# Performance work log

Hardware: AMD Instinct MI355X
Metric: run time of the kernel (lower is better)

The kernel has to match this reference:

```python
import jax, jax.numpy as jnp
import numpy as np

OT_GAMMA = 1.0
OT_EPS = 1e-06
OT_ITER = 20
L2_EPS = 1e-12  # F.normalize default eps


def _forward(ft, fs):
    # X = cat(ft, fs): [2n, d]
    X = jnp.concatenate([ft, fs], axis=0)
    # cosine similarity (F.normalize p=2 along dim=1, then X Xn^T)
    Xn = X / jnp.maximum(jnp.linalg.norm(X, axis=1, keepdims=True), L2_EPS)
    C = Xn @ Xn.T  # [2n, 2n]
    n = C.shape[0] // 2
    M = C[:n, n:]  # teacher-student cross block [n, n]
    # zscore_normalize (torch.std is unbiased -> ddof=1)
    M = (M - M.mean()) / jnp.std(M, ddof=1)

    # sinkhorn(1 - M[None], gamma, eps, maxiters), logspace=False, r=c=None
    Mb = (1.0 - M)[None, :, :]  # [1, n, n]
    B, H, W = Mb.shape
    r = 1.0 / H
    c = 1.0 / W
    P0 = jnp.exp(-OT_GAMMA * (Mb - jnp.min(Mb, axis=2, keepdims=True)))

    def step(carry, _):
        P, done = carry
        alpha = P.sum(axis=2, keepdims=True)        # [B, H, 1]
        P1 = P / alpha * r                          # row-normalize
        beta = P1.sum(axis=1, keepdims=True)        # [B, 1, W]
        new_done = done | (jnp.max(jnp.abs(beta - c)) <= OT_EPS)
        # torch breaks AFTER row-normalization when converged
        P2 = jnp.where(new_done, P1, P1 / beta * c)
        P_next = jnp.where(done, P, P2)             # freeze once converged
        return (P_next, new_done), None

    (P, _), _ = jax.lax.scan(step, (P0, jnp.array(False)), None, length=OT_ITER)
    P = P[0]  # squeeze batch -> [n, n]

    # doubly_normalize
    P = P / P.sum(axis=1, keepdims=True)
    P = P / P.sum(axis=0, keepdims=True)

    # torch.norm(A, 2) with no dim flattens -> Frobenius norm
    I = jnp.eye(P.shape[1], dtype=P.dtype)
    loss_ot = jnp.linalg.norm(P - I)
    return loss_ot, P, M


def setup_inputs() -> dict:
    key = jax.random.key(0)
    k1, k2 = jax.random.split(key)
    ft = jax.random.normal(k1, (4096, 1024), dtype=jnp.float32)
    fs = jax.random.normal(k2, (4096, 1024), dtype=jnp.float32)
    return {"ft": ft, "fs": fs}


def reference(ft, fs):
    return _forward(ft, fs)
```

## Files before the change

### kernel.cpp

```cpp
#include <hip/hip_runtime.h>
#include <stdint.h>
#include <math.h>


#define NN 4096
#define DIM 1024
#define OT_ITERS 20
#define OT_EPS_F 1e-6f
#define RC (1.0f/4096.0f)
#define RPB 16
#define SBT 512

typedef __bf16 bf16_t;
typedef _Float16 half_t;
typedef __bf16 bf16x8 __attribute__((ext_vector_type(8)));
typedef _Float16 halfx8 __attribute__((ext_vector_type(8)));
typedef float floatx4 __attribute__((ext_vector_type(4)));

typedef __attribute__((address_space(1))) void gv_t;
typedef __attribute__((address_space(3))) void lv_t;

__device__ __forceinline__ void gld_lds16(const void* g, void* lds_uniform) {
  uint32_t loff = (uint32_t)(uintptr_t)lds_uniform;
  loff = (uint32_t)__builtin_amdgcn_readfirstlane((int)loff);
  __builtin_amdgcn_global_load_lds((gv_t*)(uintptr_t)g, (lv_t*)(uintptr_t)loff, 16, 0, 0);
}

__device__ __forceinline__ void gbar(uint32_t* bar, uint32_t g) {
  __syncthreads();
  if (threadIdx.x == 0) {
    uint32_t* cnt = bar + ((blockIdx.x >> 5) * 64);
    uint32_t* root = bar + 512;
    uint32_t* gen = bar + 576;
    if (__hip_atomic_fetch_add(cnt, 1u, __ATOMIC_RELEASE, __HIP_MEMORY_SCOPE_AGENT) == 31u) {
      __hip_atomic_store(cnt, 0u, __ATOMIC_RELAXED, __HIP_MEMORY_SCOPE_AGENT);
      if (__hip_atomic_fetch_add(root, 1u, __ATOMIC_ACQ_REL, __HIP_MEMORY_SCOPE_AGENT) == 7u) {
        __hip_atomic_store(root, 0u, __ATOMIC_RELAXED, __HIP_MEMORY_SCOPE_AGENT);
        __hip_atomic_store(gen, g, __ATOMIC_RELEASE, __HIP_MEMORY_SCOPE_AGENT);
      }
    }
    while (__hip_atomic_load(gen, __ATOMIC_RELAXED, __HIP_MEMORY_SCOPE_AGENT) < g)
      __builtin_amdgcn_s_sleep(1);
    __builtin_amdgcn_fence(__ATOMIC_ACQUIRE, "agent");
  }
  __syncthreads();
}

__global__ __launch_bounds__(256) void norm_rows2(const float* __restrict__ ft,
                                                  const float* __restrict__ fs,
                                                  bf16_t* __restrict__ A,
                                                  bf16_t* __restrict__ B,
                                                  uint32_t* __restrict__ bar) {
  int gb = blockIdx.x;
  const float* X = (gb < 1024) ? ft : fs;
  bf16_t* Y = (gb < 1024) ? A : B;
  int bb = gb & 1023;
  int tid = threadIdx.x;
  int wave = tid >> 6, lane = tid & 63;
  int row = bb * 4 + wave;
  const float* xr = X + (size_t)row * DIM;
  float xv[16];
  float ss = 0.f;
#pragma unroll
  for (int k = 0; k < 16; k++) { xv[k] = xr[lane + 64 * k]; ss += xv[k] * xv[k]; }
#pragma unroll
  for (int off = 1; off < 64; off <<= 1) ss += __shfl_xor(ss, off, 64);
  float inv = rsqrtf(ss);
  bf16_t* yr = Y + (size_t)row * DIM;
#pragma unroll
  for (int k = 0; k < 16; k++) yr[lane + 64 * k] = (bf16_t)(xv[k] * inv);
  if (gb == 0) {
    for (int i = tid; i < 640; i += 256) bar[i] = 0u;
  }
}

__global__ __launch_bounds__(256) void gemm_bt(const bf16_t* __restrict__ A,
                                               const bf16_t* __restrict__ B,
                                               float* __restrict__ C,
                                               float* __restrict__ sumArr,
                                               float* __restrict__ sqArr,
                                               float* __restrict__ rmPart) {
  __shared__ __align__(16) bf16_t As[2][128 * 32];
  __shared__ __align__(16) bf16_t Bs[2][128 * 32];
  __shared__ float sred[8];
  int tid = threadIdx.x;
  int wave = tid >> 6, lane = tid & 63;
  int quad = lane >> 4, l16 = lane & 15;
  int bm = blockIdx.y, bn = blockIdx.x;
  int waveM = wave >> 1, waveN = wave & 1;
  floatx4 acc[4][4] = {};

  auto stage = [&](int k0, int buf) {
#pragma unroll
    for (int t = 0; t < 2; t++) {
      int cbase = t * 256 + wave * 64;
      int c = cbase + lane;
      int row = c >> 2, kc = c & 3;
      gld_lds16(A + (size_t)(bm * 128 + row) * DIM + (k0 + kc * 8),
                (char*)&As[buf][0] + (size_t)cbase * 16);
      gld_lds16(B + (size_t)(bn * 128 + row) * DIM + (k0 + kc * 8),
                (char*)&Bs[buf][0] + (size_t)cbase * 16);
    }
  };

  stage(0, 0);
  asm volatile("s_waitcnt vmcnt(0)" ::: "memory");
  __builtin_amdgcn_s_barrier();
  int cur = 0;
  for (int k0 = 0; k0 < DIM; k0 += 32) {
    if (k0 + 32 < DIM) stage(k0 + 32, cur ^ 1);
    bf16x8 af[4], bfr[4];
#pragma unroll
    for (int mt = 0; mt < 4; mt++)
      af[mt] = *(const bf16x8*)(&As[cur][0] + (waveM * 64 + mt * 16 + l16) * 32 + quad * 8);
#pragma unroll
    for (int nt = 0; nt < 4; nt++)
      bfr[nt] = *(const bf16x8*)(&Bs[cur][0] + (waveN * 64 + nt * 16 + l16) * 32 + quad * 8);
#pragma unroll
    for (int mt = 0; mt < 4; mt++)
#pragma unroll
      for (int nt = 0; nt < 4; nt++)
        acc[mt][nt] = __builtin_amdgcn_mfma_f32_16x16x32_bf16(af[mt], bfr[nt], acc[mt][nt], 0, 0, 0);
    asm volatile("s_waitcnt vmcnt(0)" ::: "memory");
    __builtin_amdgcn_s_barrier();
    cur ^= 1;
  }

  float lsum = 0.f, lsq = 0.f;
#pragma unroll
  for (int mt = 0; mt < 4; mt++) {
#pragma unroll
    for (int r = 0; r < 4; r++) {
      int gi = bm * 128 + waveM * 64 + mt * 16 + quad * 4 + r;
      float rmax = -3.4e38f;
#pragma unroll
      for (int nt = 0; nt < 4; nt++) {
        float vv = acc[mt][nt][r];
        int gj = bn * 128 + waveN * 64 + nt * 16 + l16;
        C[(size_t)gi * NN + gj] = vv;
        lsum += vv;
        lsq += vv * vv;
        rmax = fmaxf(rmax, vv);
      }
#pragma unroll
      for (int off = 1; off < 16; off <<= 1) rmax = fmaxf(rmax, __shfl_xor(rmax, off, 64));
      if (l16 == 0) rmPart[(size_t)(bn * 2 + waveN) * NN + gi] = rmax;
    }
  }
#pragma unroll
  for (int off = 1; off < 64; off <<= 1) {
    lsum += __shfl_xor(lsum, off, 64);
    lsq += __shfl_xor(lsq, off, 64);
  }
  if (lane == 0) { sred[wave] = lsum; sred[4 + wave] = lsq; }
  __syncthreads();
  if (tid == 0) {
    int bid = bm * 32 + bn;
    sumArr[bid] = sred[0] + sred[1] + sred[2] + sred[3];
    sqArr[bid] = sred[4] + sred[5] + sred[6] + sred[7];
  }
}

__global__ __launch_bounds__(256) void row_stats(const float* __restrict__ sumArr,
                                                 const float* __restrict__ sqArr,
                                                 const float* __restrict__ rmPart,
                                                 float* __restrict__ rowmax,
                                                 float* __restrict__ scal) {
  int tid = threadIdx.x;
  int row = blockIdx.x * 256 + tid;
  float rm = -3.4e38f;
#pragma unroll 8
  for (int p = 0; p < 64; p++) rm = fmaxf(rm, rmPart[(size_t)p * NN + row]);
  rowmax[row] = rm;
  if (blockIdx.x == 0) {
    double ds = (double)sumArr[tid] + (double)sumArr[tid + 256] +
                (double)sumArr[tid + 512] + (double)sumArr[tid + 768];
    double dq = (double)sqArr[tid] + (double)sqArr[tid + 256] +
                (double)sqArr[tid + 512] + (double)sqArr[tid + 768];
#pragma unroll
    for (int off = 1; off < 64; off <<= 1) {
      ds += __shfl_xor(ds, off, 64);
      dq += __shfl_xor(dq, off, 64);
    }
    __shared__ double dr[8];
    int wave = tid >> 6, lane = tid & 63;
    if (lane == 0) { dr[wave] = ds; dr[4 + wave] = dq; }
    __syncthreads();
    if (tid == 0) {
      double sum = dr[0] + dr[1] + dr[2] + dr[3];
      double sumsq = dr[4] + dr[5] + dr[6] + dr[7];
      double Nd = (double)NN * (double)NN;
      double meand = sum / Nd;
      double var = (sumsq - sum * sum / Nd) / (Nd - 1.0);
      scal[2] = (float)meand;
      scal[3] = (float)(1.0 / sqrt(var));
    }
  }
}

__global__ __launch_bounds__(SBT, 2) void sinkhorn_full(
    float* __restrict__ Mraw,
    float* __restrict__ Mstd,
    const float* __restrict__ scal,
    const float* __restrict__ rowmax,
    float* __restrict__ u,
    float* __restrict__ t,
    float* __restrict__ s,
    float* __restrict__ lossArr,
    uint32_t* __restrict__ bar,
    float* __restrict__ out) {
  __shared__ float red[8 * RPB];
  __shared__ float u_lds[RPB];
  __shared__ float rowmax_l[RPB];
  __shared__ float mdred[8];

  const int b = blockIdx.x;
  const int tid = threadIdx.x;
  const int wave = tid >> 6, lane = tid & 63;
  const int g0 = b * RPB;
  const int c0 = tid * 8;
  const int r0 = tid * 8;
  uint32_t bg = 0;
  const float mean = scal[2], istd = scal[3];

  halfx8 kcol[16];
  {
    float rmx[8];
    *(float4*)&rmx[0] = *(const float4*)(rowmax + r0);
    *(float4*)&rmx[4] = *(const float4*)(rowmax + r0 + 4);
#pragma unroll
    for (int rl = 0; rl < 8; rl++) {
      const float* mr = Mraw + (size_t)(r0 + rl) * NN + g0;
      float v16[16];
      *(float4*)&v16[0] = *(const float4*)(mr);
      *(float4*)&v16[4] = *(const float4*)(mr + 4);
      *(float4*)&v16[8] = *(const float4*)(mr + 8);
      *(float4*)&v16[12] = *(const float4*)(mr + 12);
      float rm = rmx[rl];
      halfx8 lo, hi;
#pragma unroll
      for (int q = 0; q < 8; q++) {
        lo[q] = (half_t)__expf((v16[q] - rm) * istd);
        hi[q] = (half_t)__expf((v16[8 + q] - rm) * istd);
      }
      kcol[rl * 2] = lo;
      kcol[rl * 2 + 1] = hi;
    }
  }

  if (tid < RPB) rowmax_l[tid] = rowmax[g0 + tid];
  __syncthreads();
  halfx8 kreg[RPB];
#pragma unroll
  for (int i = 0; i < RPB; i++) {
    float rm = rowmax_l[i];
    const float* mr = Mraw + (size_t)(g0 + i) * NN + c0;
    float* mo = Mstd + (size_t)(g0 + i) * NN + c0;
    float4 a = *(const float4*)mr;
    float4 bb = *(const float4*)(mr + 4);
    float4 sa, sb;
    sa.x = (a.x - mean) * istd;  sa.y = (a.y - mean) * istd;
    sa.z = (a.z - mean) * istd;  sa.w = (a.w - mean) * istd;
    sb.x = (bb.x - mean) * istd; sb.y = (bb.y - mean) * istd;
    sb.z = (bb.z - mean) * istd; sb.w = (bb.w - mean) * istd;
    *(float4*)mo = sa;
    *(float4*)(mo + 4) = sb;
    halfx8 kp;
    kp[0] = (half_t)__expf((a.x - rm) * istd);
    kp[1] = (half_t)__expf((a.y - rm) * istd);
    kp[2] = (half_t)__expf((a.z - rm) * istd);
    kp[3] = (half_t)__expf((a.w - rm) * istd);
    kp[4] = (half_t)__expf((bb.x - rm) * istd);
    kp[5] = (half_t)__expf((bb.y - rm) * istd);
    kp[6] = (half_t)__expf((bb.z - rm) * istd);
    kp[7] = (half_t)__expf((bb.w - rm) * istd);
    kreg[i] = kp;
  }

  float vr[8];
#pragma unroll
  for (int q = 0; q < 8; q++) vr[q] = 1.0f;

  auto row_phase = [&](float scale, bool toLds) {
    float part[RPB];
#pragma unroll
    for (int i = 0; i < RPB; i++) {
      float p = 0.f;
#pragma unroll
      for (int q = 0; q < 8; q++) p += (float)kreg[i][q] * vr[q];
      part[i] = p;
    }
#pragma unroll
    for (int off = 1; off < 64; off <<= 1)
#pragma unroll
      for (int i = 0; i < RPB; i++) part[i] += __shfl_xor(part[i], off, 64);
    if (lane == 0) {
#pragma unroll
      for (int i = 0; i < RPB; i++) red[wave * RPB + i] = part[i];
    }
    __syncthreads();
    if (tid < RPB) {
      float dsum = 0.f;
#pragma unroll
      for (int w = 0; w < 8; w++) dsum += red[w * RPB + tid];
      float uv = scale / dsum;
      u[g0 + tid] = uv;
      if (toLds) u_lds[tid] = uv;
    }
  };

  auto col_phase = [&](float* dst) {
    float u8[8];
    *(float4*)&u8[0] = *(const float4*)(u + r0);
    *(float4*)&u8[4] = *(const float4*)(u + r0 + 4);
    float tp[RPB];
#pragma unroll
    for (int j = 0; j < RPB; j++) tp[j] = 0.f;
#pragma unroll
    for (int rl = 0; rl < 8; rl++) {
      float uv = u8[rl];
#pragma unroll
      for (int q = 0; q < 8; q++) {
        tp[q] += (float)kcol[rl * 2][q] * uv;
        tp[8 + q] += (float)kcol[rl * 2 + 1][q] * uv;
      }
    }
#pragma unroll
    for (int off = 1; off < 64; off <<= 1)
#pragma unroll
      for (int j = 0; j < RPB; j++) tp[j] += __shfl_xor(tp[j], off, 64);
    if (lane == 0) {
#pragma unroll
      for (int j = 0; j < RPB; j++) red[wave * RPB + j] = tp[j];
    }
    __syncthreads();
    if (tid < RPB) {
      float tv = 0.f;
#pragma unroll
      for (int w = 0; w < 8; w++) tv += red[w * RPB + tid];
      dst[g0 + tid] = tv;
    }
  };

  auto mdcheck = [&](float* t8) -> float {
    *(float4*)&t8[0] = *(const float4*)(t + c0);
    *(float4*)&t8[4] = *(const float4*)(t + c0 + 4);
    float dev = 0.f;
#pragma unroll
    for (int q = 0; q < 8; q++) dev = fmaxf(dev, fabsf(vr[q] * t8[q] - RC));
#pragma unroll
    for (int off = 1; off < 64; off <<= 1) dev = fmaxf(dev, __shfl_xor(dev, off, 64));
    if (lane == 0) mdred[wave] = dev;
    __syncthreads();
    float md = mdred[0];
#pragma unroll
    for (int w = 1; w < 8; w++) md = fmaxf(md, mdred[w]);
    __syncthreads();
    return md;
  };

  bool frozen = false;
  for (int it = 0; it < OT_ITERS; it++) {
    if (it > 0) {
      float t8[8];
      float md = mdcheck(t8);
      if (md <= OT_EPS_F) { frozen = true; break; }
#pragma unroll
      for (int q = 0; q < 8; q++) vr[q] = RC / t8[q];
    }
    row_phase(RC, false);
    gbar(bar, ++bg);
    col_phase(t);
    gbar(bar, ++bg);
  }
  if (!frozen) {
    float t8[8];
    float md = mdcheck(t8);
    if (md > OT_EPS_F) {
#pragma unroll
      for (int q = 0; q < 8; q++) vr[q] = RC / t8[q];
    }
  }

  row_phase(1.0f, true);
  gbar(bar, ++bg);
  col_phase(s);
  gbar(bar, ++bg);

  float s8[8];
  *(float4*)&s8[0] = *(const float4*)(s + c0);
  *(float4*)&s8[4] = *(const float4*)(s + c0 + 4);
  float isv[8];
#pragma unroll
  for (int q = 0; q < 8; q++) isv[q] = 1.0f / s8[q];
  float ls = 0.f;
#pragma unroll
  for (int i = 0; i < RPB; i++) {
    int gi = g0 + i;
    float wi = u_lds[i];
    float* prow = Mraw + (size_t)gi * NN + c0;
    float4 pa, pb;
    float pv[8];
#pragma unroll
    for (int q = 0; q < 8; q++) {
      float p = (float)kreg[i][q] * wi * isv[q];
      pv[q] = p;
      float d = p - ((gi == c0 + q) ? 1.0f : 0.0f);
      ls += d * d;
    }
    pa.x = pv[0]; pa.y = pv[1]; pa.z = pv[2]; pa.w = pv[3];
    pb.x = pv[4]; pb.y = pv[5]; pb.z = pv[6]; pb.w = pv[7];
    *(float4*)prow = pa;
    *(float4*)(prow + 4) = pb;
  }
#pragma unroll
  for (int off = 1; off < 64; off <<= 1) ls += __shfl_xor(ls, off, 64);
  if (lane == 0) red[wave] = ls;
  __syncthreads();
  if (tid == 0) {
    float tot = 0.f;
#pragma unroll
    for (int w = 0; w < 8; w++) tot += red[w];
    lossArr[b] = tot;
  }
  gbar(bar, ++bg);
  if (b == 0) {
    float lv = (tid < 256) ? lossArr[tid] : 0.f;
#pragma unroll
    for (int off = 1; off < 64; off <<= 1) lv += __shfl_xor(lv, off, 64);
    if (lane == 0) mdred[wave] = lv;
    __syncthreads();
    if (tid == 0) {
      float tot = 0.f;
#pragma unroll
      for (int w = 0; w < 8; w++) tot += mdred[w];
      out[0] = sqrtf(tot);
    }
  }
}

extern "C" void kernel_launch(void* const* d_in, const int* in_sizes, int n_in, void* d_out,
                              int out_size, void* d_ws, size_t ws_size, hipStream_t stream) {
  const float* ft = (const float*)d_in[0];
  const float* fs = (const float*)d_in[1];
  float* out = (float*)d_out;

  char* ws = (char*)d_ws;
  bf16_t* A = (bf16_t*)ws;
  bf16_t* B = (bf16_t*)(ws + (8u << 20));
  float* fbase = (float*)(ws + (16u << 20));
  float* u = fbase;
  float* t = fbase + 4096;
  float* s = fbase + 8192;
  float* rowmax = fbase + 12288;
  float* scal = fbase + 16384;
  float* lossArr = fbase + 16640;
  uint32_t* bar = (uint32_t*)(fbase + 17408);
  float* sumArr = fbase + 18432;
  float* sqArr = fbase + 19456;
  float* rmPart = fbase + 20480;

  float* P_slot = out + 1;
  float* M_slot = out + 1 + (size_t)NN * NN;

  norm_rows2<<<2048, 256, 0, stream>>>(ft, fs, A, B, bar);
  gemm_bt<<<dim3(32, 32), 256, 0, stream>>>(A, B, P_slot, sumArr, sqArr, rmPart);
  row_stats<<<16, 256, 0, stream>>>(sumArr, sqArr, rmPart, rowmax, scal);
  sinkhorn_full<<<256, SBT, 0, stream>>>(P_slot, M_slot, scal, rowmax, u, t, s,
                                         lossArr, bar, out);
}
```

Before: 411.0 us.

## Split grid barrier generation flags, remap sinkhorn strips, write raw GEMM to workspace

The grid barrier now writes the release generation to eight separate cache-line-spaced flags, and each group of 32 blocks polls its own flag, so the spinning is spread over several lines. Sinkhorn blocks are remapped to strips interleaved by block index mod 8, which changes which strips land on which XCD. When the workspace is large enough, the raw GEMM output goes to a separate workspace buffer instead of the P output slot, so the kernel no longer reads and overwrites the same buffer. Vector float4 stores are replaced with scalar stores, which may reduce store coalescing efficiency.

```diff
diff --git a/kernel.cpp b/kernel.cpp
--- a/kernel.cpp
+++ b/kernel.cpp
@@ -29,17 +29,20 @@
 __device__ __forceinline__ void gbar(uint32_t* bar, uint32_t g) {
   __syncthreads();
   if (threadIdx.x == 0) {
-    uint32_t* cnt = bar + ((blockIdx.x >> 5) * 64);
+    int grp = blockIdx.x >> 5;
+    uint32_t* cnt = bar + grp * 64;
     uint32_t* root = bar + 512;
-    uint32_t* gen = bar + 576;
     if (__hip_atomic_fetch_add(cnt, 1u, __ATOMIC_RELEASE, __HIP_MEMORY_SCOPE_AGENT) == 31u) {
       __hip_atomic_store(cnt, 0u, __ATOMIC_RELAXED, __HIP_MEMORY_SCOPE_AGENT);
       if (__hip_atomic_fetch_add(root, 1u, __ATOMIC_ACQ_REL, __HIP_MEMORY_SCOPE_AGENT) == 7u) {
         __hip_atomic_store(root, 0u, __ATOMIC_RELAXED, __HIP_MEMORY_SCOPE_AGENT);
-        __hip_atomic_store(gen, g, __ATOMIC_RELEASE, __HIP_MEMORY_SCOPE_AGENT);
+#pragma unroll
+        for (int q = 0; q < 8; q++)
+          __hip_atomic_store(bar + 576 + q * 64, g, __ATOMIC_RELEASE, __HIP_MEMORY_SCOPE_AGENT);
       }
     }
-    while (__hip_atomic_load(gen, __ATOMIC_RELAXED, __HIP_MEMORY_SCOPE_AGENT) < g)
+    uint32_t* mygen = bar + 576 + grp * 64;
+    while (__hip_atomic_load(mygen, __ATOMIC_RELAXED, __HIP_MEMORY_SCOPE_AGENT) < g)
       __builtin_amdgcn_s_sleep(1);
     __builtin_amdgcn_fence(__ATOMIC_ACQUIRE, "agent");
   }
@@ -70,7 +73,7 @@
 #pragma unroll
   for (int k = 0; k < 16; k++) yr[lane + 64 * k] = (bf16_t)(xv[k] * inv);
   if (gb == 0) {
-    for (int i = tid; i < 640; i += 256) bar[i] = 0u;
+    for (int i = tid; i < 1088; i += 256) bar[i] = 0u;
   }
 }
 
@@ -199,7 +202,8 @@
 }
 
 __global__ __launch_bounds__(SBT, 2) void sinkhorn_full(
-    float* __restrict__ Mraw,
+    const float* __restrict__ Mraw,
+    float* __restrict__ Pout,
     float* __restrict__ Mstd,
     const float* __restrict__ scal,
     const float* __restrict__ rowmax,
@@ -217,7 +221,8 @@
   const int b = blockIdx.x;
   const int tid = threadIdx.x;
   const int wave = tid >> 6, lane = tid & 63;
-  const int g0 = b * RPB;
+  const int strip = (b & 7) * 32 + (b >> 3);
+  const int g0 = strip * RPB;
   const int c0 = tid * 8;
   const int r0 = tid * 8;
   uint32_t bg = 0;
@@ -258,13 +263,10 @@
     float* mo = Mstd + (size_t)(g0 + i) * NN + c0;
     float4 a = *(const float4*)mr;
     float4 bb = *(const float4*)(mr + 4);
-    float4 sa, sb;
-    sa.x = (a.x - mean) * istd;  sa.y = (a.y - mean) * istd;
-    sa.z = (a.z - mean) * istd;  sa.w = (a.w - mean) * istd;
-    sb.x = (bb.x - mean) * istd; sb.y = (bb.y - mean) * istd;
-    sb.z = (bb.z - mean) * istd; sb.w = (bb.w - mean) * istd;
-    *(float4*)mo = sa;
-    *(float4*)(mo + 4) = sb;
+    mo[0] = (a.x - mean) * istd;  mo[1] = (a.y - mean) * istd;
+    mo[2] = (a.z - mean) * istd;  mo[3] = (a.w - mean) * istd;
+    mo[4] = (bb.x - mean) * istd; mo[5] = (bb.y - mean) * istd;
+    mo[6] = (bb.z - mean) * istd; mo[7] = (bb.w - mean) * istd;
     halfx8 kp;
     kp[0] = (half_t)__expf((a.x - rm) * istd);
     kp[1] = (half_t)__expf((a.y - rm) * istd);
@@ -398,20 +400,14 @@
   for (int i = 0; i < RPB; i++) {
     int gi = g0 + i;
     float wi = u_lds[i];
-    float* prow = Mraw + (size_t)gi * NN + c0;
-    float4 pa, pb;
-    float pv[8];
+    float* prow = Pout + (size_t)gi * NN + c0;
 #pragma unroll
     for (int q = 0; q < 8; q++) {
       float p = (float)kreg[i][q] * wi * isv[q];
-      pv[q] = p;
+      prow[q] = p;
       float d = p - ((gi == c0 + q) ? 1.0f : 0.0f);
       ls += d * d;
     }
-    pa.x = pv[0]; pa.y = pv[1]; pa.z = pv[2]; pa.w = pv[3];
-    pb.x = pv[4]; pb.y = pv[5]; pb.z = pv[6]; pb.w = pv[7];
-    *(float4*)prow = pa;
-    *(float4*)(prow + 4) = pb;
   }
 #pragma unroll
   for (int off = 1; off < 64; off <<= 1) ls += __shfl_xor(ls, off, 64);
@@ -455,7 +451,7 @@
   float* rowmax = fbase + 12288;
   float* scal = fbase + 16384;
   float* lossArr = fbase + 16640;
-  uint32_t* bar = (uint32_t*)(fbase + 17408);
+  uint32_t* bar = (uint32_t*)(fbase + 16896);
   float* sumArr = fbase + 18432;
   float* sqArr = fbase + 19456;
   float* rmPart = fbase + 20480;
@@ -463,9 +459,11 @@
   float* P_slot = out + 1;
   float* M_slot = out + 1 + (size_t)NN * NN;
 
+  float* Mws = (ws_size >= (96ull << 20)) ? (float*)(ws + (32u << 20)) : P_slot;
+
   norm_rows2<<<2048, 256, 0, stream>>>(ft, fs, A, B, bar);
-  gemm_bt<<<dim3(32, 32), 256, 0, stream>>>(A, B, P_slot, sumArr, sqArr, rmPart);
+  gemm_bt<<<dim3(32, 32), 256, 0, stream>>>(A, B, Mws, sumArr, sqArr, rmPart);
   row_stats<<<16, 256, 0, stream>>>(sumArr, sqArr, rmPart, rowmax, scal);
-  sinkhorn_full<<<256, SBT, 0, stream>>>(P_slot, M_slot, scal, rowmax, u, t, s,
+  sinkhorn_full<<<256, SBT, 0, stream>>>(Mws, P_slot, M_slot, scal, rowmax, u, t, s,
                                          lossArr, bar, out);
 }
```

Result: no change. 406.4 us (-1.1%).
